# Performance work log

Hardware: AMD Instinct MI355X
Metric: run time of the kernel (lower is better)

Reference implementation:

```python
import jax, jax.numpy as jnp
import numpy as np

NH, NL, NP, GA = 8, 4, 4, 8  # num_heads, num_levels, num_points, grid_align_num
SHAPES = np.array([[128, 128], [64, 64], [32, 32], [16, 16]], dtype=np.int64)  # (W, H) per level


def _grid_sample(img, grid):
    """F.grid_sample bilinear, padding_mode='zeros', align_corners=False.
    img: [N,C,H,W], grid: [N,Hg,Wg,2] in [-1,1] (x,y). Returns [N,C,Hg,Wg]."""
    N, C, H, W = img.shape
    x = (grid[..., 0] + 1.0) * (W * 0.5) - 0.5
    y = (grid[..., 1] + 1.0) * (H * 0.5) - 0.5
    x0 = jnp.floor(x)
    y0 = jnp.floor(y)
    wx = (x - x0)[:, None]  # [N,1,Hg,Wg]
    wy = (y - y0)[:, None]
    x0i = x0.astype(jnp.int32)
    y0i = y0.astype(jnp.int32)
    img_flat = img.reshape(N, C, H * W)
    Hg, Wg = grid.shape[1], grid.shape[2]

    def tap(ix, iy):
        valid = (ix >= 0) & (ix < W) & (iy >= 0) & (iy < H)
        lin = jnp.clip(iy, 0, H - 1) * W + jnp.clip(ix, 0, W - 1)
        v = jnp.take_along_axis(img_flat, lin.reshape(N, 1, Hg * Wg), axis=2)
        return v.reshape(N, C, Hg, Wg) * valid[:, None].astype(img.dtype)

    v00 = tap(x0i, y0i)
    v01 = tap(x0i + 1, y0i)
    v10 = tap(x0i, y0i + 1)
    v11 = tap(x0i + 1, y0i + 1)
    return (v00 * (1 - wx) * (1 - wy) + v01 * wx * (1 - wy)
            + v10 * (1 - wx) * wy + v11 * wx * wy)


def setup_inputs() -> dict:
    key = jax.random.key(0)
    ks = jax.random.split(key, 6)
    bs, nq, E = 2, 16384, 256
    total = int((SHAPES[:, 0] * SHAPES[:, 1]).sum())  # 21760
    query = jax.random.normal(ks[0], (bs, nq, E), jnp.float32)
    value = jax.random.normal(ks[1], (bs, total, NH, E // NH), jnp.float32)
    reference_points = jax.random.uniform(ks[2], (bs, nq, 1, NL * 2), jnp.float32)
    W_off = jax.random.normal(ks[3], (NH * NL * NP * 2, E), jnp.float32) * 0.01
    # structured offset bias per init_weights (directional rays, radius ~ point index)
    thetas = jnp.arange(NH, dtype=jnp.float32) * (2.0 * np.pi / NH)
    gi = jnp.stack([jnp.cos(thetas), jnp.sin(thetas)], -1)  # [NH,2]
    gi = gi / jnp.max(jnp.abs(gi), axis=-1, keepdims=True)
    gi = jnp.tile(gi[:, None, None, :], (1, NL, NP, 1))
    gi = gi * jnp.arange(1, NP + 1, dtype=jnp.float32)[None, None, :, None]
    b_off = gi.reshape(-1)
    W_attn = jax.random.normal(ks[4], (NH * NL * NP, E), jnp.float32) * 0.01
    b_attn = jax.random.normal(ks[5], (NH * NL * NP,), jnp.float32) * 0.01
    return {"query": query, "value": value, "reference_points": reference_points,
            "W_off": W_off, "b_off": b_off, "W_attn": W_attn, "b_attn": b_attn,
            "spatial_shapes": np.asarray(SHAPES)}


def reference(query, value, reference_points, W_off, b_off, W_attn, b_attn, spatial_shapes):
    bs, nq, E = query.shape
    d = E // NH
    shapes = np.asarray(spatial_shapes)  # static [L,2] (W,H)

    # sampling offsets and locations (non-deploy path)
    off = (query @ W_off.T + b_off).reshape(bs, nq, NH, NL * NP * 2)
    ref = jnp.tile(reference_points, (1, 1, NH, NP)).reshape(bs, nq, NH, NL * NP * 2)
    # offset_normalizer: (1/spatial_shapes).repeat(1, NP).flatten() -> layout (l, p, xy)
    norm = jnp.asarray(np.tile(1.0 / shapes.astype(np.float32), (1, NP)).reshape(-1))
    loc = (ref + off * norm) * 2.0 - 1.0  # [bs, nq, NH, NL*NP*2]

    # attention weights: softmax over levels*points, regrouped to (L, G, P) layout
    attn = jax.nn.softmax((query @ W_attn.T + b_attn).reshape(bs, nq, NH, NL * NP), axis=-1)
    attn = (attn.reshape(bs, nq // GA, GA, NH, NL, NP)
            .transpose(0, 3, 1, 4, 2, 5)
            .reshape(bs * NH, 1, nq // GA, NL * GA * NP))

    grids = loc.reshape(bs, nq, NH, NL, NP, 2)
    outs = []
    start = 0
    for lvl in range(NL):
        W_, H_ = int(shapes[lvl, 0]), int(shapes[lvl, 1])
        n = H_ * W_
        v = value[:, start:start + n].transpose(0, 2, 3, 1).reshape(bs * NH, d, H_, W_)
        start += n
        g = grids[:, :, :, lvl].transpose(0, 2, 1, 3, 4).reshape(bs * NH, nq // GA, GA * NP, 2)
        outs.append(_grid_sample(v, g))  # [bs*NH, d, nq//GA, GA*NP]
    samp = jnp.concatenate(outs, axis=-1) * attn  # [bs*NH, d, nq//GA, NL*GA*NP]
    # reduce_sum linear with fixed 0/1 weight == sum over levels and points per group slot
    out = samp.reshape(bs * NH, d, nq // GA, NL, GA, NP).sum(axis=(3, 5))
    return out.reshape(bs, NH * d, nq)
```

## Files before the change

kernel.cpp:

```cpp
#include <hip/hip_runtime.h>
#include <hip/hip_bf16.h>


typedef __attribute__((ext_vector_type(4))) float    float4v;
typedef __attribute__((ext_vector_type(8))) _Float16 half8;
typedef __attribute__((ext_vector_type(4))) _Float16 half4;
typedef __attribute__((ext_vector_type(2))) _Float16 half2v;

#define NQ    16384
#define NTOK  21760
#define LREC  48

#define GEMM_BLOCKS 768
#define CONV_GRID   2048
#define CONV_N4     2785280

union H8 { half8 v; half2v p[4]; };

#define LDSTR 88
__global__ __launch_bounds__(256) void gemm_kernel(
    const float* __restrict__ qf,
    const float* __restrict__ Woff, const float* __restrict__ Wattn,
    const float* __restrict__ boff, const float* __restrict__ battn,
    _Float16* __restrict__ lh) {
  const int tid = threadIdx.x;

  __shared__ _Float16 As[128 * LDSTR];
  __shared__ _Float16 Bs[128 * LDSTR];

  const int lane = tid & 63;
  const int wv   = tid >> 6;
  const int wm   = wv >> 1, wn = wv & 1;
  const int quad = lane >> 4;
  const int r    = lane & 15;
  const int blockM = (blockIdx.x & 255) * 128;
  const int n0     = (blockIdx.x >> 8) * 128;

  float4v acc[4][4];
#pragma unroll
  for (int i = 0; i < 4; ++i)
#pragma unroll
    for (int j = 0; j < 4; ++j) acc[i][j] = (float4v){0.f, 0.f, 0.f, 0.f};

  for (int kc = 0; kc < 4; ++kc) {
    const int k0 = kc * 64;
    if (kc) __syncthreads();
#pragma unroll
    for (int it = 0; it < 8; ++it) {
      int idx = it * 256 + tid;
      int row = idx >> 4, k4 = idx & 15;
      float4v v = *(const float4v*)(qf + (size_t)(blockM + row) * 256 + k0 + k4 * 4);
      half4 o;
      o[0] = (_Float16)v[0]; o[1] = (_Float16)v[1];
      o[2] = (_Float16)v[2]; o[3] = (_Float16)v[3];
      *(half4*)&As[row * LDSTR + k4 * 4] = o;
    }
#pragma unroll
    for (int it = 0; it < 8; ++it) {
      int idx = it * 256 + tid;
      int row = idx >> 4, k4 = idx & 15;
      int n = n0 + row;
      const float* src = (n < 256) ? (Woff + (size_t)n * 256)
                                   : (Wattn + (size_t)(n - 256) * 256);
      float4v v = *(const float4v*)(src + k0 + k4 * 4);
      half4 o;
      o[0] = (_Float16)v[0]; o[1] = (_Float16)v[1];
      o[2] = (_Float16)v[2]; o[3] = (_Float16)v[3];
      *(half4*)&Bs[row * LDSTR + k4 * 4] = o;
    }
    __syncthreads();

#pragma unroll
    for (int kf = 0; kf < 2; ++kf) {
      const int ko = kf * 32 + quad * 8;
      half8 af[4], bf[4];
#pragma unroll
      for (int mi = 0; mi < 4; ++mi)
        af[mi] = *(const half8*)&As[(wm * 64 + mi * 16 + r) * LDSTR + ko];
#pragma unroll
      for (int ni = 0; ni < 4; ++ni)
        bf[ni] = *(const half8*)&Bs[(wn * 64 + ni * 16 + r) * LDSTR + ko];
#pragma unroll
      for (int mi = 0; mi < 4; ++mi)
#pragma unroll
        for (int ni = 0; ni < 4; ++ni)
          acc[mi][ni] = __builtin_amdgcn_mfma_f32_16x16x32_f16(af[mi], bf[ni], acc[mi][ni], 0, 0, 0);
    }
  }

#pragma unroll
  for (int mi = 0; mi < 4; ++mi) {
    const int mb = blockM + wm * 64 + mi * 16 + quad * 4;
#pragma unroll
    for (int ni = 0; ni < 4; ++ni) {
      const int n = n0 + wn * 64 + ni * 16 + r;
      const float bias = (n < 256) ? boff[n] : battn[n - 256];
      const int h    = (n < 256) ? (n >> 5) : ((n - 256) >> 4);
      const int slot = (n < 256) ? (n & 31) : (32 + ((n - 256) & 15));
#pragma unroll
      for (int reg = 0; reg < 4; ++reg) {
        const int bq = mb + reg;
        const int b = bq >> 14, q = bq & 16383;
        lh[((size_t)(b * 8 + h) * NQ + q) * LREC + slot] =
            (_Float16)(acc[mi][ni][reg] + bias);
      }
    }
  }
}

__global__ __launch_bounds__(256) void conv_kernel(
    const float* __restrict__ val, _Float16* __restrict__ vh) {
  for (int i = blockIdx.x * 256 + threadIdx.x; i < CONV_N4;
       i += CONV_GRID * 256) {
    float4v v = ((const float4v*)val)[i];
    half4 o;
    o[0] = (_Float16)v[0]; o[1] = (_Float16)v[1];
    o[2] = (_Float16)v[2]; o[3] = (_Float16)v[3];
    ((half4*)vh)[i] = o;
  }
}

__global__ __launch_bounds__(256) void sample_kernel(
    const _Float16* __restrict__ vh, const float* __restrict__ refp,
    const _Float16* __restrict__ lh, float* __restrict__ out) {
  const int bid   = blockIdx.x;
  const int xcd   = bid & 7;
  const int local = bid >> 3;
  const int hb    = xcd * 2 + (local >> 10);
  const int qt    = local & 1023;
  const int h     = hb & 7;
  const int b     = hb >> 3;
  const int tid = threadIdx.x;

  __shared__ _Float16 wsm[16][16];
  {
    const int q16  = tid >> 4;
    const int slot = tid & 15;
    const float lg = (float)lh[((size_t)hb * NQ + qt * 16 + q16) * LREC + 32 + slot];
    float m = lg;
    m = fmaxf(m, __shfl_xor(m, 1));
    m = fmaxf(m, __shfl_xor(m, 2));
    m = fmaxf(m, __shfl_xor(m, 4));
    m = fmaxf(m, __shfl_xor(m, 8));
    const float e = __expf(lg - m);
    float s = e;
    s += __shfl_xor(s, 1);
    s += __shfl_xor(s, 2);
    s += __shfl_xor(s, 4);
    s += __shfl_xor(s, 8);
    wsm[q16][slot] = (_Float16)(e * (1.0f / s));
  }
  __syncthreads();

  const int c4 = tid & 3;
  const int l  = (tid >> 2) & 3;
  const int qi = tid >> 4;
  const int q  = qt * 16 + qi;
  const size_t bq = (size_t)b * NQ + q;
  const _Float16* rec = lh + ((size_t)hb * NQ + q) * LREC;

  const half8 oh = *(const half8*)(rec + l * 8);
  const half4 ownw = *(const half4*)&wsm[qi][l * 4];

  float4v rp0 = *(const float4v*)(refp + bq * 8);
  float4v rp1 = *(const float4v*)(refp + bq * 8 + 4);
  const float rpx[4] = {rp0[0], rp0[2], rp1[0], rp1[2]};
  const float rpy[4] = {rp0[1], rp0[3], rp1[1], rp1[3]};

  const int   W    = 128 >> l;
  const float fW   = (float)W;
  const int   base = (l == 0) ? 0 : (l == 1) ? 16384 : (l == 2) ? 20480 : 21504;
  const _Float16* vlev = vh + (size_t)b * NTOK * 256 + h * 32 + c4 * 8
                            + (size_t)base * 256;

  half2v accl0 = (half2v){(_Float16)0, (_Float16)0};
  half2v accl1 = (half2v){(_Float16)0, (_Float16)0};
  half2v accl2 = (half2v){(_Float16)0, (_Float16)0};
  half2v accl3 = (half2v){(_Float16)0, (_Float16)0};

#pragma unroll
  for (int p = 0; p < 4; ++p) {
    const float a  = (float)ownw[p];
    const float ox = (float)oh[p * 2];
    const float oy = (float)oh[p * 2 + 1];
    const float x = rpx[p] * fW + ox - 0.5f;
    const float y = rpy[p] * fW + oy - 0.5f;
    const float xf = floorf(x), yf = floorf(y);
    const float fx = x - xf, fy = y - yf;
    const int ix = (int)xf, iy = (int)yf;
    const int ix0 = min(max(ix, 0), W - 1);
    const int ix1 = min(max(ix + 1, 0), W - 1);
    const int iy0 = min(max(iy, 0), W - 1);
    const int iy1 = min(max(iy + 1, 0), W - 1);
    const float wx0 = ((unsigned)ix       < (unsigned)W) ? 1.f - fx : 0.f;
    const float wx1 = ((unsigned)(ix + 1) < (unsigned)W) ? fx       : 0.f;
    const float wy0 = ((unsigned)iy       < (unsigned)W) ? 1.f - fy : 0.f;
    const float wy1 = ((unsigned)(iy + 1) < (unsigned)W) ? fy       : 0.f;
    const _Float16 w00 = (_Float16)(a * wx0 * wy0);
    const _Float16 w01 = (_Float16)(a * wx1 * wy0);
    const _Float16 w10 = (_Float16)(a * wx0 * wy1);
    const _Float16 w11 = (_Float16)(a * wx1 * wy1);
    const half2v h00 = (half2v){w00, w00};
    const half2v h01 = (half2v){w01, w01};
    const half2v h10 = (half2v){w10, w10};
    const half2v h11 = (half2v){w11, w11};
    const _Float16* r0 = vlev + (size_t)(iy0 * W) * 256;
    const _Float16* r1 = vlev + (size_t)(iy1 * W) * 256;
    H8 t00, t01, t10, t11;
    t00.v = *(const half8*)(r0 + ix0 * 256);
    t01.v = *(const half8*)(r0 + ix1 * 256);
    t10.v = *(const half8*)(r1 + ix0 * 256);
    t11.v = *(const half8*)(r1 + ix1 * 256);
    accl0 += h00 * t00.p[0] + h01 * t01.p[0] + h10 * t10.p[0] + h11 * t11.p[0];
    accl1 += h00 * t00.p[1] + h01 * t01.p[1] + h10 * t10.p[1] + h11 * t11.p[1];
    accl2 += h00 * t00.p[2] + h01 * t01.p[2] + h10 * t10.p[2] + h11 * t11.p[2];
    accl3 += h00 * t00.p[3] + h01 * t01.p[3] + h10 * t10.p[3] + h11 * t11.p[3];
  }

  float acc0[4], acc1[4];
  acc0[0] = (float)accl0[0]; acc0[1] = (float)accl0[1];
  acc0[2] = (float)accl1[0]; acc0[3] = (float)accl1[1];
  acc1[0] = (float)accl2[0]; acc1[1] = (float)accl2[1];
  acc1[2] = (float)accl3[0]; acc1[3] = (float)accl3[1];

  __shared__ float sm[4][16][33];
#pragma unroll
  for (int j = 0; j < 4; ++j) {
    sm[l][qi][c4 * 8 + j]     = acc0[j];
    sm[l][qi][c4 * 8 + 4 + j] = acc1[j];
  }
  __syncthreads();
  const size_t obase = ((size_t)b * 256 + h * 32) * NQ + qt * 16;
#pragma unroll
  for (int i = 0; i < 2; ++i) {
    const int idx = i * 256 + tid;
    const int c  = idx >> 4;
    const int ql = idx & 15;
    const float v = ((sm[0][ql][c] + sm[1][ql][c]) + sm[2][ql][c]) + sm[3][ql][c];
    out[obase + (size_t)c * NQ + ql] = v;
  }
}

extern "C" void kernel_launch(void* const* d_in, const int* in_sizes, int n_in,
                              void* d_out, int out_size, void* d_ws, size_t ws_size,
                              hipStream_t stream) {
  const float* query = (const float*)d_in[0];
  const float* value = (const float*)d_in[1];
  const float* refp  = (const float*)d_in[2];
  const float* Woff  = (const float*)d_in[3];
  const float* boff  = (const float*)d_in[4];
  const float* Wattn = (const float*)d_in[5];
  const float* battn = (const float*)d_in[6];
  float* out = (float*)d_out;

  char* ws = (char*)d_ws;
  _Float16* vh = (_Float16*)ws;
  _Float16* lh = (_Float16*)(ws + 22282240);

  gemm_kernel<<<GEMM_BLOCKS, 256, 0, stream>>>(
      query, Woff, Wattn, boff, battn, lh);
  conv_kernel<<<CONV_GRID, 256, 0, stream>>>(value, vh);
  sample_kernel<<<16384, 256, 0, stream>>>(vh, refp, lh, out);
}
```

Measured before the change: 218.8 us.

## Repack fp16 value tensor head-major with XCD-aware conversion blocks

The conversion kernel now writes the fp16 value tensor in a per-(batch, head) contiguous layout [b*h][token][32] instead of the original token-major interleaved layout. Block indices are mapped so each XCD converts the same head slices that its sample blocks later read. The sample kernel's bilinear gathers stride 64 bytes per token instead of 512, which packs neighbouring pixels densely and is meant to improve cache locality and L2 reuse per XCD. The conversion kernel now reads strided 32-float chunks per token, which may coalesce slightly less well on the read side.

After: 203.0 us. 1.08x faster.

```diff
diff --git a/kernel.cpp b/kernel.cpp
--- a/kernel.cpp
+++ b/kernel.cpp
@@ -12,8 +12,7 @@
 #define LREC  48
 
 #define GEMM_BLOCKS 768
-#define CONV_GRID   2048
-#define CONV_N4     2785280
+#define CONV_BLOCKS 5440
 
 union H8 { half8 v; half2v p[4]; };
 
@@ -110,14 +109,26 @@
 
 __global__ __launch_bounds__(256) void conv_kernel(
     const float* __restrict__ val, _Float16* __restrict__ vh) {
-  for (int i = blockIdx.x * 256 + threadIdx.x; i < CONV_N4;
-       i += CONV_GRID * 256) {
-    float4v v = ((const float4v*)val)[i];
-    half4 o;
-    o[0] = (_Float16)v[0]; o[1] = (_Float16)v[1];
-    o[2] = (_Float16)v[2]; o[3] = (_Float16)v[3];
-    ((half4*)vh)[i] = o;
-  }
+  const int bid   = blockIdx.x;
+  const int xcd   = bid & 7;
+  const int local = bid >> 3;
+  const int sl    = (local >= 340) ? 1 : 0;
+  const int hb    = xcd * 2 + sl;
+  const int tokT  = local - sl * 340;
+  const int tid   = threadIdx.x;
+  const int c8    = tid & 3;
+  const int tok   = tokT * 64 + (tid >> 2);
+  const int b     = hb >> 3, h = hb & 7;
+
+  const float* src = val + ((size_t)b * NTOK + tok) * 256 + h * 32 + c8 * 8;
+  float4v v0 = *(const float4v*)src;
+  float4v v1 = *(const float4v*)(src + 4);
+  half8 o;
+  o[0] = (_Float16)v0[0]; o[1] = (_Float16)v0[1];
+  o[2] = (_Float16)v0[2]; o[3] = (_Float16)v0[3];
+  o[4] = (_Float16)v1[0]; o[5] = (_Float16)v1[1];
+  o[6] = (_Float16)v1[2]; o[7] = (_Float16)v1[3];
+  *(half8*)(vh + ((size_t)hb * NTOK + tok) * 32 + c8 * 8) = o;
 }
 
 __global__ __launch_bounds__(256) void sample_kernel(
@@ -170,8 +181,7 @@
   const int   W    = 128 >> l;
   const float fW   = (float)W;
   const int   base = (l == 0) ? 0 : (l == 1) ? 16384 : (l == 2) ? 20480 : 21504;
-  const _Float16* vlev = vh + (size_t)b * NTOK * 256 + h * 32 + c4 * 8
-                            + (size_t)base * 256;
+  const _Float16* vlev = vh + ((size_t)hb * NTOK + base) * 32 + c4 * 8;
 
   half2v accl0 = (half2v){(_Float16)0, (_Float16)0};
   half2v accl1 = (half2v){(_Float16)0, (_Float16)0};
@@ -204,13 +214,13 @@
     const half2v h01 = (half2v){w01, w01};
     const half2v h10 = (half2v){w10, w10};
     const half2v h11 = (half2v){w11, w11};
-    const _Float16* r0 = vlev + (size_t)(iy0 * W) * 256;
-    const _Float16* r1 = vlev + (size_t)(iy1 * W) * 256;
+    const _Float16* r0 = vlev + (size_t)(iy0 * W) * 32;
+    const _Float16* r1 = vlev + (size_t)(iy1 * W) * 32;
     H8 t00, t01, t10, t11;
-    t00.v = *(const half8*)(r0 + ix0 * 256);
-    t01.v = *(const half8*)(r0 + ix1 * 256);
-    t10.v = *(const half8*)(r1 + ix0 * 256);
-    t11.v = *(const half8*)(r1 + ix1 * 256);
+    t00.v = *(const half8*)(r0 + ix0 * 32);
+    t01.v = *(const half8*)(r0 + ix1 * 32);
+    t10.v = *(const half8*)(r1 + ix0 * 32);
+    t11.v = *(const half8*)(r1 + ix1 * 32);
     accl0 += h00 * t00.p[0] + h01 * t01.p[0] + h10 * t10.p[0] + h11 * t11.p[0];
     accl1 += h00 * t00.p[1] + h01 * t01.p[1] + h10 * t10.p[1] + h11 * t11.p[1];
     accl2 += h00 * t00.p[2] + h01 * t01.p[2] + h10 * t10.p[2] + h11 * t11.p[2];
@@ -259,6 +269,6 @@
 
   gemm_kernel<<<GEMM_BLOCKS, 256, 0, stream>>>(
       query, Woff, Wattn, boff, battn, lh);
-  conv_kernel<<<CONV_GRID, 256, 0, stream>>>(value, vh);
+  conv_kernel<<<CONV_BLOCKS, 256, 0, stream>>>(value, vh);
   sample_kernel<<<16384, 256, 0, stream>>>(vh, refp, lh, out);
 }
```
